# Kernel tuning notes

Measured on AMD Instinct MI355X. Metric: run time of the kernel, lower is better.

Reference implementation:

```python
import jax, jax.numpy as jnp
import numpy as np

N = 50000        # num_nodes
E = 800000       # num edges (avg degree 16)
R = 8            # num_relations
D_IN = 128       # input_dim
D_H = 128        # gnn_dim
D_OUT = 128      # embed_dim
NUM_DRUGS = 4000 # nodes with node_type == 0 used for pairing
P = 8192         # number of drug pairs (edge_filter columns)


def setup_inputs() -> dict:
    key = jax.random.key(0)
    ks = jax.random.split(key, 24)
    s = 0.05

    def w(k, shape):
        return jax.random.normal(k, shape, jnp.float32) * s

    inp = {
        "x": jax.random.normal(ks[0], (N, D_IN), jnp.float32),
        "edge_index": jax.random.randint(ks[1], (2, E), 0, N),
        "edge_type": jax.random.randint(ks[2], (E,), 0, R),
        "node_type": jax.random.randint(ks[3], (N,), 0, 2),
        "edge_filter": jax.random.randint(ks[4], (2, P), 0, NUM_DRUGS),
        # RGCN layer 1/2/3: per-relation weights, root weight, bias
        "W1": w(ks[5], (R, D_IN, D_H)), "root1": w(ks[6], (D_IN, D_H)), "b1": jnp.zeros((D_H,), jnp.float32),
        "W2": w(ks[7], (R, D_H, D_H)),  "root2": w(ks[8], (D_H, D_H)),  "b2": jnp.zeros((D_H,), jnp.float32),
        "W3": w(ks[9], (R, D_H, D_H)),  "root3": w(ks[10], (D_H, D_H)), "b3": jnp.zeros((D_H,), jnp.float32),
        # ComboMLP: Bilinear(d,d,d) + 3-layer MLP
        "bil_W": w(ks[11], (D_H, D_H, D_H)), "bil_b": jnp.zeros((D_H,), jnp.float32),
        "m1_W": w(ks[12], (D_H, D_H)), "m1_b": jnp.zeros((D_H,), jnp.float32),
        "m2_W": w(ks[13], (D_H, D_H)), "m2_b": jnp.zeros((D_H,), jnp.float32),
        "m3_W": w(ks[14], (D_H, D_OUT)), "m3_b": jnp.zeros((D_OUT,), jnp.float32),
    }
    return inp


def _rgcn_layer(x, src, dst, etype, W, root, b):
    # PyG RGCNConv with aggr='mean': per relation r, mean of neighbor
    # features over incoming rel-r edges, transformed by W[r]; plus root + bias.
    d = x.shape[1]
    msgs = x[src]                                   # [E, d] gather
    seg = dst * R + etype                           # per-(node, relation) segment id
    agg = jax.ops.segment_sum(msgs, seg, num_segments=N * R).reshape(N, R, d)
    cnt = jax.ops.segment_sum(jnp.ones_like(etype, jnp.float32), seg,
                              num_segments=N * R).reshape(N, R, 1)
    mean = agg / jnp.maximum(cnt, 1.0)              # nodes w/o rel-r edges -> 0
    return jnp.einsum('nrd,rde->ne', mean, W) + x @ root + b


def reference(x, edge_index, edge_type, node_type, edge_filter,
              W1, root1, b1, W2, root2, b2, W3, root3, b3,
              bil_W, bil_b, m1_W, m1_b, m2_W, m2_b, m3_W, m3_b):
    src, dst = edge_index[0], edge_index[1]
    h = jax.nn.relu(_rgcn_layer(x, src, dst, edge_type, W1, root1, b1))
    h = jax.nn.relu(_rgcn_layer(h, src, dst, edge_type, W2, root2, b2))
    h = jax.nn.relu(_rgcn_layer(h, src, dst, edge_type, W3, root3, b3))

    # drug_embeds = kg_out[where(node_type == 0)] (fixed-size for jit)
    drug_idx = jnp.nonzero(node_type == 0, size=NUM_DRUGS, fill_value=0)[0]
    drug = h[drug_idx]                              # [NUM_DRUGS, d]
    fa = drug[edge_filter[0]]                       # [P, d]
    fb = drug[edge_filter[1]]                       # [P, d]

    # torch.nn.Bilinear: out[p,o] = fa[p] @ bil_W[o] @ fb[p] + bil_b[o]
    x_ab = jax.nn.relu(jnp.einsum('pi,oij,pj->po', fa, bil_W, fb) + bil_b)
    x_ab = jax.nn.relu(x_ab @ m1_W + m1_b)
    x_ab = jax.nn.relu(x_ab @ m2_W + m2_b)
    return x_ab @ m3_W + m3_b                       # [P, D_OUT]
```

## Files before the change

kernel.cpp:

```cpp
#include <hip/hip_runtime.h>
#include <hip/hip_bf16.h>

typedef unsigned short ushort_t;
typedef __attribute__((ext_vector_type(8))) short short8v;
typedef __attribute__((ext_vector_type(4))) float f32x4;
typedef __attribute__((ext_vector_type(4))) int int4v;

#define NN 50000
#define EE 800000
#define RRR 8
#define DD 128
#define NDRUG 4000
#define PPAIR 8192
#define BML 32
#define AFS 1160

#define XB4   (NN * DD / 4)
#define WCAT1 (144 * 128 * 8)
#define PREP_T (XB4 + 3 * WCAT1 + 3 * 16384 + 2097152)

__device__ __forceinline__ float bf2f(ushort_t u) {
    unsigned int v = ((unsigned int)u) << 16;
    float f; __builtin_memcpy(&f, &v, 4); return f;
}
__device__ __forceinline__ ushort_t f2bf(float f) {
    unsigned int b; __builtin_memcpy(&b, &f, 4);
    unsigned int r = (b + 0x7FFFu + ((b >> 16) & 1u)) >> 16;
    return (ushort_t)r;
}
__device__ __forceinline__ unsigned int pkbf(float lo, float hi) {
    unsigned int r;
    asm("v_cvt_pk_bf16_f32 %0, %1, %2" : "=v"(r) : "v"(lo), "v"(hi));
    return r;
}

__global__ __launch_bounds__(256) void k_prep(
        const float* __restrict__ x,
        const float* __restrict__ W1, const float* __restrict__ r1,
        const float* __restrict__ W2, const float* __restrict__ r2,
        const float* __restrict__ W3, const float* __restrict__ r3,
        const float* __restrict__ m1W, const float* __restrict__ m2W,
        const float* __restrict__ m3W, const float* __restrict__ bilW,
        const int* __restrict__ ei, const int* __restrict__ et,
        ushort_t* __restrict__ xb,
        ushort_t* __restrict__ Wc1, ushort_t* __restrict__ Wc2, ushort_t* __restrict__ Wc3,
        ushort_t* __restrict__ mo1, ushort_t* __restrict__ mo2, ushort_t* __restrict__ mo3,
        ushort_t* __restrict__ Wb3, int* __restrict__ cnt) {
    int idx = blockIdx.x * 256 + threadIdx.x;
    if (idx < XB4) {
        float4 v = ((const float4*)x)[idx];
        uint2 o;
        o.x = (unsigned int)f2bf(v.x) | ((unsigned int)f2bf(v.y) << 16);
        o.y = (unsigned int)f2bf(v.z) | ((unsigned int)f2bf(v.w) << 16);
        ((uint2*)xb)[idx] = o;
    } else if (idx < XB4 + 3 * WCAT1) {
        int t = idx - XB4;
        int l = t / WCAT1, j = t - l * WCAT1;
        const float* W8   = (l == 0) ? W1 : (l == 1) ? W2 : W3;
        const float* root = (l == 0) ? r1 : (l == 1) ? r2 : r3;
        ushort_t* dst     = (l == 0) ? Wc1 : (l == 1) ? Wc2 : Wc3;
        int e = j & 7, col = (j >> 3) & 127, ko = j >> 10;
        int k = ko * 8 + e, slab = k >> 7, kk = k & 127;
        const float* src = (slab < 8) ? (W8 + slab * 16384) : root;
        dst[j] = f2bf(src[kk * 128 + col]);
    } else if (idx < XB4 + 3 * WCAT1 + 3 * 16384) {
        int t = idx - XB4 - 3 * WCAT1;
        int l = t >> 14, j = t & 16383;
        const float* src = (l == 0) ? m1W : (l == 1) ? m2W : m3W;
        ushort_t* dst    = (l == 0) ? mo1 : (l == 1) ? mo2 : mo3;
        int col = j >> 7, kk = j & 127;
        dst[j] = f2bf(src[kk * 128 + col]);
    } else if (idx < PREP_T) {
        int j = idx - (XB4 + 3 * WCAT1 + 3 * 16384);
        int e = j & 7, o = (j >> 3) & 127, ko = j >> 10;
        Wb3[j] = f2bf(bilW[(size_t)o * 16384 + ko * 8 + e]);
    } else {
        int e = idx - PREP_T;
        if (e < EE) {
            int dst = ei[EE + e];
            atomicAdd(&cnt[dst * RRR + et[e]], 1);
        }
    }
}

__global__ __launch_bounds__(1024) void k_scanA(const int* __restrict__ cnt,
                                                const int* __restrict__ ntype,
                                                float* __restrict__ inv,
                                                int* __restrict__ offs,
                                                int* __restrict__ selx,
                                                int* __restrict__ part,
                                                int* __restrict__ part2) {
    __shared__ int w1[16], w2[16];
    int tid = threadIdx.x, wid = tid >> 6, lane = tid & 63;
    int i = blockIdx.x * 1024 + tid;
    int a0 = 0, b0 = 0;
    if (i < NN) {
#pragma unroll
        for (int r = 0; r < RRR; r++) {
            int c = cnt[i * RRR + r];
            a0 += c;
            inv[i * RRR + r] = 1.0f / (float)(c > 0 ? c : 1);
        }
        b0 = (ntype[i] == 0) ? 1 : 0;
    }
    int a = a0, b = b0;
#pragma unroll
    for (int off = 1; off < 64; off <<= 1) {
        int ua = __shfl_up(a, off);
        int ub = __shfl_up(b, off);
        if (lane >= off) { a += ua; b += ub; }
    }
    if (lane == 63) { w1[wid] = a; w2[wid] = b; }
    __syncthreads();
    if (wid == 0) {
        int wa = (lane < 16) ? w1[lane] : 0;
        int wb = (lane < 16) ? w2[lane] : 0;
#pragma unroll
        for (int off = 1; off < 16; off <<= 1) {
            int ua = __shfl_up(wa, off);
            int ub = __shfl_up(wb, off);
            if (lane >= off) { wa += ua; wb += ub; }
        }
        if (lane < 16) { w1[lane] = wa; w2[lane] = wb; }
    }
    __syncthreads();
    if (i < NN) {
        offs[i] = (wid ? w1[wid - 1] : 0) + (a - a0);
        selx[i] = (wid ? w2[wid - 1] : 0) + (b - b0);
    }
    if (tid == 0) { part[blockIdx.x] = w1[15]; part2[blockIdx.x] = w2[15]; }
}

__global__ __launch_bounds__(64) void k_scanB(int* __restrict__ part,
                                              int* __restrict__ part2, int nPart) {
    int tid = threadIdx.x;
    int p0 = (tid < nPart) ? part[tid] : 0;
    int q0 = (tid < nPart) ? part2[tid] : 0;
    int p = p0, q = q0;
#pragma unroll
    for (int off = 1; off < 64; off <<= 1) {
        int u = __shfl_up(p, off);
        int v = __shfl_up(q, off);
        if (tid >= off) { p += u; q += v; }
    }
    if (tid < nPart) { part[tid] = p - p0; part2[tid] = q - q0; }
}

__global__ __launch_bounds__(1024) void k_scanC(int* __restrict__ offs,
                                                const int* __restrict__ selx,
                                                const int* __restrict__ part,
                                                const int* __restrict__ part2,
                                                const int* __restrict__ ntype,
                                                int* __restrict__ cursor,
                                                int* __restrict__ didx) {
    int i = blockIdx.x * 1024 + threadIdx.x;
    if (i < NN) {
        int v = offs[i] + part[blockIdx.x];
        offs[i] = v;
        cursor[i] = v;
        if (ntype[i] == 0) {
            int s = selx[i] + part2[blockIdx.x];
            if (s < NDRUG) didx[s] = i;
        }
    }
    if (i == NN) offs[NN] = EE;
}

__global__ __launch_bounds__(256) void k_scatter(const int* __restrict__ ei,
                                                 const int* __restrict__ et,
                                                 int* __restrict__ cursor,
                                                 int* __restrict__ sorted) {
    int e = blockIdx.x * 256 + threadIdx.x;
    if (e < EE) {
        int dst = ei[EE + e];
        int pos = atomicAdd(&cursor[dst], 1);
        sorted[pos] = ei[e] | (et[e] << 20);
    }
}

__global__ __launch_bounds__(512) void k_layer(const ushort_t* __restrict__ hin,
                                               const ushort_t* __restrict__ WcatT,
                                               const float* __restrict__ bias,
                                               const float* __restrict__ inv,
                                               const int* __restrict__ offs,
                                               const int* __restrict__ sorted,
                                               ushort_t* __restrict__ hout) {
    __shared__ short Af[BML * AFS];
    int tid = threadIdx.x;
    int n0 = blockIdx.x * BML;
    int node = tid >> 4, tsub = tid & 15;
    int n = n0 + node;

    float acc[8][8];
#pragma unroll
    for (int r = 0; r < 8; r++)
#pragma unroll
        for (int q = 0; q < 8; q++) acc[r][q] = 0.f;
    short8v hv = {0, 0, 0, 0, 0, 0, 0, 0};

    if (n < NN) {
        hv = ((const short8v*)hin)[(size_t)n * 16 + tsub];
        int e0 = offs[n], e1 = offs[n + 1];
        const int4v* hg = (const int4v*)hin;
        for (int e = e0; e < e1; e++) {
            int pk = sorted[e];
            int src = pk & 0xFFFFF;
            int et = pk >> 20;
            union { int4v v; short s[8]; } u;
            u.v = hg[(size_t)src * 16 + tsub];
            float v[8];
#pragma unroll
            for (int q = 0; q < 8; q++) v[q] = bf2f((ushort_t)u.s[q]);
#define CASE_R(R) case R: _Pragma("unroll") for (int q = 0; q < 8; q++) acc[R][q] += v[q]; break;
            switch (et) {
                CASE_R(0) CASE_R(1) CASE_R(2) CASE_R(3)
                CASE_R(4) CASE_R(5) CASE_R(6) CASE_R(7)
            }
#undef CASE_R
        }
    }
    int nc = (n < NN) ? n : (NN - 1);
#pragma unroll
    for (int slab = 0; slab < 8; slab++) {
        float sc = (n < NN) ? inv[nc * 8 + slab] : 0.f;
        union { unsigned int u[4]; short8v v; } cv;
        cv.u[0] = pkbf(acc[slab][0] * sc, acc[slab][1] * sc);
        cv.u[1] = pkbf(acc[slab][2] * sc, acc[slab][3] * sc);
        cv.u[2] = pkbf(acc[slab][4] * sc, acc[slab][5] * sc);
        cv.u[3] = pkbf(acc[slab][6] * sc, acc[slab][7] * sc);
        *(short8v*)&Af[node * AFS + slab * 128 + tsub * 8] = cv.v;
    }
    *(short8v*)&Af[node * AFS + 1024 + tsub * 8] = hv;
    __syncthreads();

    int wid = tid >> 6, lane = tid & 63, lo = lane & 15, hi = lane >> 4;
    int rhalf = wid & 1, cgrp = wid >> 1;
    int arow = rhalf * 16 + lo;
    f32x4 a0v = {0.f, 0.f, 0.f, 0.f}, a1v = {0.f, 0.f, 0.f, 0.f};
    const int4v* Bg = (const int4v*)WcatT;
#pragma unroll
    for (int kc = 0; kc < 9; kc++) {
#pragma unroll
        for (int s = 0; s < 4; s++) {
            short8v a = *(const short8v*)&Af[arow * AFS + kc * 128 + s * 32 + hi * 8];
            int ko = kc * 16 + s * 4 + hi;
            union { int4v i; short8v s8; } b0, b1;
            b0.i = Bg[ko * 128 + cgrp * 32 + lo];
            b1.i = Bg[ko * 128 + cgrp * 32 + 16 + lo];
            a0v = __builtin_amdgcn_mfma_f32_16x16x32_bf16(a, b0.s8, a0v, 0, 0, 0);
            a1v = __builtin_amdgcn_mfma_f32_16x16x32_bf16(a, b1.s8, a1v, 0, 0, 0);
        }
    }
#pragma unroll
    for (int q = 0; q < 4; q++) {
        int r = n0 + rhalf * 16 + hi * 4 + q;
        if (r < NN) {
            int c = cgrp * 32 + lo;
            float v0 = fmaxf(a0v[q] + bias[c], 0.f);
            float v1 = fmaxf(a1v[q] + bias[c + 16], 0.f);
            hout[(size_t)r * 128 + c] = f2bf(v0);
            hout[(size_t)r * 128 + c + 16] = f2bf(v1);
        }
    }
}

__global__ __launch_bounds__(256) void k_mfma_nn(const ushort_t* __restrict__ A,
                                                 const ushort_t* __restrict__ Wt,
                                                 const float* __restrict__ bias,
                                                 ushort_t* __restrict__ outb,
                                                 float* __restrict__ outf,
                                                 int M, int nMblk, int relu) {
    __shared__ short As[64 * 136];
    __shared__ short Bs[128 * 136];
    int tid = threadIdx.x;
    int mblk = blockIdx.x % nMblk;
    int row0 = mblk * 64;

    const int4v* Ag = (const int4v*)A;
    int4v* AsV = (int4v*)As;
    for (int idx = tid; idx < 1024; idx += 256) {
        int row = idx >> 4, ck = idx & 15;
        int grow = row0 + row;
        int4v v = {0, 0, 0, 0};
        if (grow < M) v = Ag[(size_t)grow * 16 + ck];
        AsV[row * 17 + ck] = v;
    }
    const int4v* Wg = (const int4v*)Wt;
    int4v* BsV = (int4v*)Bs;
    for (int idx = tid; idx < 2048; idx += 256) {
        int col = idx >> 4, ck = idx & 15;
        BsV[col * 17 + ck] = Wg[idx];
    }
    __syncthreads();

    int wid = tid >> 6, lane = tid & 63, lo = lane & 15, hi = lane >> 4;
    int wrow0 = wid * 16;
    f32x4 acc[8];
#pragma unroll
    for (int t = 0; t < 8; t++) acc[t] = (f32x4)(0.f);

#pragma unroll
    for (int s = 0; s < 4; ++s) {
        short8v a = *(const short8v*)&As[(wrow0 + lo) * 136 + s * 32 + hi * 8];
#pragma unroll
        for (int t = 0; t < 8; t++) {
            short8v b = *(const short8v*)&Bs[(t * 16 + lo) * 136 + s * 32 + hi * 8];
            acc[t] = __builtin_amdgcn_mfma_f32_16x16x32_bf16(a, b, acc[t], 0, 0, 0);
        }
    }

#pragma unroll
    for (int t = 0; t < 8; t++) {
        int col = t * 16 + lo;
        float bs = bias ? bias[col] : 0.f;
#pragma unroll
        for (int q = 0; q < 4; q++) {
            int grow = row0 + wrow0 + hi * 4 + q;
            if (grow < M) {
                float v = acc[t][q] + bs;
                if (relu) v = fmaxf(v, 0.f);
                size_t oidx = (size_t)grow * 128 + col;
                if (outb) outb[oidx] = f2bf(v);
                else      outf[oidx] = v;
            }
        }
    }
}

__global__ __launch_bounds__(512) void k_bil(const ushort_t* __restrict__ hb,
                                             const int* __restrict__ didx,
                                             const int* __restrict__ efil,
                                             const ushort_t* __restrict__ Wb,
                                             const float* __restrict__ bilb,
                                             ushort_t* __restrict__ xab) {
    __shared__ __align__(16) char smem[67072];
    __shared__ int pa[64], pb[64];
    float* faT = (float*)smem;
    float* fbF = (float*)(smem + 33280);
    int tid = threadIdx.x;
    int p0 = blockIdx.x * 64;

    if (tid < 64) pa[tid] = didx[efil[p0 + tid]];
    else if (tid < 128) pb[tid - 64] = didx[efil[PPAIR + p0 + tid - 64]];
    __syncthreads();

    for (int t = tid; t < 1024; t += 512) {
        int p = t >> 4, c8 = t & 15;
        const int4v* hg = (const int4v*)hb;
        union { int4v v; short s[8]; } ra, rb;
        ra.v = hg[(size_t)pa[p] * 16 + c8];
        rb.v = hg[(size_t)pb[p] * 16 + c8];
        float4* fb4 = (float4*)fbF;
        float4 f0, f1;
        f0.x = bf2f((ushort_t)rb.s[0]); f0.y = bf2f((ushort_t)rb.s[1]);
        f0.z = bf2f((ushort_t)rb.s[2]); f0.w = bf2f((ushort_t)rb.s[3]);
        f1.x = bf2f((ushort_t)rb.s[4]); f1.y = bf2f((ushort_t)rb.s[5]);
        f1.z = bf2f((ushort_t)rb.s[6]); f1.w = bf2f((ushort_t)rb.s[7]);
        fb4[p * 33 + c8 * 2] = f0;
        fb4[p * 33 + c8 * 2 + 1] = f1;
#pragma unroll
        for (int j = 0; j < 8; j++)
            faT[(c8 * 8 + j) * 65 + p] = bf2f((ushort_t)ra.s[j]);
    }
    __syncthreads();

    int wid = tid >> 6, lane = tid & 63, lo = lane & 15, hi = lane >> 4;
    int ph = wid & 1, kQ = wid >> 1;
    const int4v* Wbg = (const int4v*)Wb;
    const float4* fb4 = (const float4*)fbF;

    f32x4 acc0[8], acc1[8];
#pragma unroll
    for (int t = 0; t < 8; t++) { acc0[t] = (f32x4)(0.f); acc1[t] = (f32x4)(0.f); }

    for (int s = 0; s < 128; ++s) {
        int ko = (kQ << 9) + (s << 2) + hi;
        int4v braw[8];
#pragma unroll
        for (int t = 0; t < 8; t++)
            braw[t] = Wbg[ko * 128 + t * 16 + lo];

        int i = (kQ << 5) + (s >> 2);
        int jc4 = ((s & 3) << 3) + (hi << 1);
        short8v afr0, afr1;
#pragma unroll
        for (int mi = 0; mi < 2; ++mi) {
            int prow = (ph << 5) + (mi << 4) + lo;
            float fa = faT[i * 65 + prow];
            float4 f0 = fb4[prow * 33 + jc4];
            float4 f1 = fb4[prow * 33 + jc4 + 1];
            union { unsigned int u[4]; short8v v; } cv;
            cv.u[0] = pkbf(fa * f0.x, fa * f0.y);
            cv.u[1] = pkbf(fa * f0.z, fa * f0.w);
            cv.u[2] = pkbf(fa * f1.x, fa * f1.y);
            cv.u[3] = pkbf(fa * f1.z, fa * f1.w);
            if (mi == 0) afr0 = cv.v; else afr1 = cv.v;
        }
#pragma unroll
        for (int t = 0; t < 8; t++) {
            union { int4v i4; short8v s8; } bb; bb.i4 = braw[t];
            acc0[t] = __builtin_amdgcn_mfma_f32_16x16x32_bf16(afr0, bb.s8, acc0[t], 0, 0, 0);
            acc1[t] = __builtin_amdgcn_mfma_f32_16x16x32_bf16(afr1, bb.s8, acc1[t], 0, 0, 0);
        }
    }
    __syncthreads();

    float* redF = (float*)smem;
    if (kQ >= 2) {
        float* r = redF + (((kQ - 2) << 1) + ph) * 4096;
#pragma unroll
        for (int t = 0; t < 8; t++)
#pragma unroll
            for (int q = 0; q < 4; q++) {
                r[(hi * 4 + q) * 128 + t * 16 + lo] = acc0[t][q];
                r[(16 + hi * 4 + q) * 128 + t * 16 + lo] = acc1[t][q];
            }
    }
    __syncthreads();
    if (kQ < 2) {
        float* r = redF + ((kQ << 1) + ph) * 4096;
#pragma unroll
        for (int t = 0; t < 8; t++)
#pragma unroll
            for (int q = 0; q < 4; q++) {
                acc0[t][q] += r[(hi * 4 + q) * 128 + t * 16 + lo];
                acc1[t][q] += r[(16 + hi * 4 + q) * 128 + t * 16 + lo];
            }
    }
    __syncthreads();
    if (kQ == 1) {
        float* r = redF + ph * 4096;
#pragma unroll
        for (int t = 0; t < 8; t++)
#pragma unroll
            for (int q = 0; q < 4; q++) {
                r[(hi * 4 + q) * 128 + t * 16 + lo] = acc0[t][q];
                r[(16 + hi * 4 + q) * 128 + t * 16 + lo] = acc1[t][q];
            }
    }
    __syncthreads();
    if (kQ == 0) {
        float* r = redF + ph * 4096;
#pragma unroll
        for (int t = 0; t < 8; t++) {
            int col = t * 16 + lo;
            float bs = bilb[col];
#pragma unroll
            for (int q = 0; q < 4; q++) {
                float s0 = acc0[t][q] + r[(hi * 4 + q) * 128 + col] + bs;
                float s1 = acc1[t][q] + r[(16 + hi * 4 + q) * 128 + col] + bs;
                int pr0 = p0 + (ph << 5) + hi * 4 + q;
                int pr1 = pr0 + 16;
                xab[(size_t)pr0 * 128 + col] = f2bf(fmaxf(s0, 0.f));
                xab[(size_t)pr1 * 128 + col] = f2bf(fmaxf(s1, 0.f));
            }
        }
    }
}


extern "C" void kernel_launch(void* const* d_in, const int* in_sizes, int n_in,
                              void* d_out, int out_size, void* d_ws, size_t ws_size,
                              hipStream_t stream) {
    const float* x      = (const float*)d_in[0];
    const int*   ei     = (const int*)d_in[1];
    const int*   et     = (const int*)d_in[2];
    const int*   ntype  = (const int*)d_in[3];
    const int*   efil   = (const int*)d_in[4];
    const float* W1 = (const float*)d_in[5];
    const float* r1 = (const float*)d_in[6];
    const float* b1 = (const float*)d_in[7];
    const float* W2 = (const float*)d_in[8];
    const float* r2 = (const float*)d_in[9];
    const float* b2 = (const float*)d_in[10];
    const float* W3 = (const float*)d_in[11];
    const float* r3 = (const float*)d_in[12];
    const float* b3 = (const float*)d_in[13];
    const float* bilW = (const float*)d_in[14];
    const float* bilb = (const float*)d_in[15];
    const float* m1W = (const float*)d_in[16];
    const float* m1b = (const float*)d_in[17];
    const float* m2W = (const float*)d_in[18];
    const float* m2b = (const float*)d_in[19];
    const float* m3W = (const float*)d_in[20];
    const float* m3b = (const float*)d_in[21];
    float* outp = (float*)d_out;

    char* ws = (char*)d_ws;
    size_t off = 0;
    auto alloc = [&](size_t bytes) { size_t c = off; off = (off + bytes + 255) & ~(size_t)255; return c; };

    const int nScanBlk = (NN + 1023) / 1024;

    size_t oxb   = alloc((size_t)NN * 128 * 2);
    size_t ohA   = alloc((size_t)NN * 128 * 2);
    size_t ohB   = alloc((size_t)NN * 128 * 2);
    size_t oWc1  = alloc((size_t)WCAT1 * 2);
    size_t oWc2  = alloc((size_t)WCAT1 * 2);
    size_t oWc3  = alloc((size_t)WCAT1 * 2);
    size_t omW1  = alloc((size_t)16384 * 2);
    size_t omW2  = alloc((size_t)16384 * 2);
    size_t omW3  = alloc((size_t)16384 * 2);
    size_t oWb   = alloc((size_t)2097152 * 2);
    size_t oxab1 = alloc((size_t)PPAIR * 128 * 2);
    size_t oxab2 = alloc((size_t)PPAIR * 128 * 2);
    size_t ocnt  = alloc((size_t)NN * RRR * sizeof(int));
    size_t odidx = alloc((size_t)NDRUG * sizeof(int));
    size_t oinv  = alloc((size_t)NN * RRR * sizeof(float));
    size_t ooffs = alloc((size_t)(NN + 1) * sizeof(int));
    size_t oselx = alloc((size_t)NN * sizeof(int));
    size_t ocur  = alloc((size_t)NN * sizeof(int));
    size_t opart = alloc((size_t)64 * sizeof(int));
    size_t opart2 = alloc((size_t)64 * sizeof(int));
    size_t osort = alloc((size_t)EE * sizeof(int));

    ushort_t* xb   = (ushort_t*)(ws + oxb);
    ushort_t* hbA  = (ushort_t*)(ws + ohA);
    ushort_t* hbB  = (ushort_t*)(ws + ohB);
    ushort_t* Wc1  = (ushort_t*)(ws + oWc1);
    ushort_t* Wc2  = (ushort_t*)(ws + oWc2);
    ushort_t* Wc3  = (ushort_t*)(ws + oWc3);
    ushort_t* mWt1 = (ushort_t*)(ws + omW1);
    ushort_t* mWt2 = (ushort_t*)(ws + omW2);
    ushort_t* mWt3 = (ushort_t*)(ws + omW3);
    ushort_t* Wb3  = (ushort_t*)(ws + oWb);
    ushort_t* xab1 = (ushort_t*)(ws + oxab1);
    ushort_t* xab2 = (ushort_t*)(ws + oxab2);
    int*      cnt  = (int*)(ws + ocnt);
    int*      didx = (int*)(ws + odidx);
    float*    inv  = (float*)(ws + oinv);
    int*      offs = (int*)(ws + ooffs);
    int*      selx = (int*)(ws + oselx);
    int*      cursor = (int*)(ws + ocur);
    int*      part = (int*)(ws + opart);
    int*      part2 = (int*)(ws + opart2);
    int*      sorted = (int*)(ws + osort);

    hipMemsetAsync(cnt, 0, (odidx - ocnt) + (size_t)NDRUG * sizeof(int), stream);

    k_prep<<<(PREP_T + EE + 255) / 256, 256, 0, stream>>>(
        x, W1, r1, W2, r2, W3, r3, m1W, m2W, m3W, bilW, ei, et,
        xb, Wc1, Wc2, Wc3, mWt1, mWt2, mWt3, Wb3, cnt);

    k_scanA<<<nScanBlk, 1024, 0, stream>>>(cnt, ntype, inv, offs, selx, part, part2);
    k_scanB<<<1, 64, 0, stream>>>(part, part2, nScanBlk);
    k_scanC<<<nScanBlk + 1, 1024, 0, stream>>>(offs, selx, part, part2, ntype, cursor, didx);
    k_scatter<<<(EE + 255) / 256, 256, 0, stream>>>(ei, et, cursor, sorted);

    const int NBL = (NN + BML - 1) / BML;

    k_layer<<<NBL, 512, 0, stream>>>(xb,  Wc1, b1, inv, offs, sorted, hbA);
    k_layer<<<NBL, 512, 0, stream>>>(hbA, Wc2, b2, inv, offs, sorted, hbB);
    k_layer<<<NBL, 512, 0, stream>>>(hbB, Wc3, b3, inv, offs, sorted, hbA);

    k_bil<<<PPAIR / 64, 512, 0, stream>>>(hbA, didx, efil, Wb3, bilb, xab1);
    const int nMblkP = PPAIR / 64;
    k_mfma_nn<<<nMblkP, 256, 0, stream>>>(xab1, mWt1, m1b, xab2, nullptr, PPAIR, nMblkP, 1);
    k_mfma_nn<<<nMblkP, 256, 0, stream>>>(xab2, mWt2, m2b, xab1, nullptr, PPAIR, nMblkP, 1);
    k_mfma_nn<<<nMblkP, 256, 0, stream>>>(xab1, mWt3, m3b, nullptr, outp, PPAIR, nMblkP, 0);
}
```

Measured before the change: 719.0 us.

## Split bilinear kernel across K halves and smaller pair tiles with reduction pass

The bilinear kernel now processes 32 pairs per block instead of 64. It also splits the 16384-long reduction dimension into two halves across blocks, raising the grid from 128 to 512 blocks so more compute units are occupied. Each block reduces its 8 waves' partials in shared memory and writes fp32 partial sums to a workspace. A new elementwise kernel adds the two halves, applies bias and ReLU, and stores bf16. The cost is roughly double the bilinear weight traffic, extra fp32 partial writes and reads, and one more kernel launch.

```diff
diff --git a/kernel.cpp b/kernel.cpp
--- a/kernel.cpp
+++ b/kernel.cpp
@@ -331,21 +331,22 @@
                                              const int* __restrict__ didx,
                                              const int* __restrict__ efil,
                                              const ushort_t* __restrict__ Wb,
-                                             const float* __restrict__ bilb,
-                                             ushort_t* __restrict__ xab) {
-    __shared__ __align__(16) char smem[67072];
-    __shared__ int pa[64], pb[64];
+                                             float* __restrict__ partial) {
+    __shared__ __align__(16) char smem[65536];
+    __shared__ int pa[32], pb[32];
     float* faT = (float*)smem;
-    float* fbF = (float*)(smem + 33280);
+    float* fbF = (float*)(smem + 16896);
     int tid = threadIdx.x;
-    int p0 = blockIdx.x * 64;
-
-    if (tid < 64) pa[tid] = didx[efil[p0 + tid]];
-    else if (tid < 128) pb[tid - 64] = didx[efil[PPAIR + p0 + tid - 64]];
-    __syncthreads();
-
-    for (int t = tid; t < 1024; t += 512) {
-        int p = t >> 4, c8 = t & 15;
+    int pt = blockIdx.x & 255;
+    int kh = blockIdx.x >> 8;
+    int p0 = pt * 32;
+
+    if (tid < 32) pa[tid] = didx[efil[p0 + tid]];
+    else if (tid < 64) pb[tid - 32] = didx[efil[PPAIR + p0 + tid - 32]];
+    __syncthreads();
+
+    {
+        int p = tid >> 4, c8 = tid & 15;
         const int4v* hg = (const int4v*)hb;
         union { int4v v; short s[8]; } ra, rb;
         ra.v = hg[(size_t)pa[p] * 16 + c8];
@@ -360,12 +361,11 @@
         fb4[p * 33 + c8 * 2 + 1] = f1;
 #pragma unroll
         for (int j = 0; j < 8; j++)
-            faT[(c8 * 8 + j) * 65 + p] = bf2f((ushort_t)ra.s[j]);
+            faT[(c8 * 8 + j) * 33 + p] = bf2f((ushort_t)ra.s[j]);
     }
     __syncthreads();
 
     int wid = tid >> 6, lane = tid & 63, lo = lane & 15, hi = lane >> 4;
-    int ph = wid & 1, kQ = wid >> 1;
     const int4v* Wbg = (const int4v*)Wb;
     const float4* fb4 = (const float4*)fbF;
 
@@ -373,20 +373,20 @@
 #pragma unroll
     for (int t = 0; t < 8; t++) { acc0[t] = (f32x4)(0.f); acc1[t] = (f32x4)(0.f); }
 
-    for (int s = 0; s < 128; ++s) {
-        int ko = (kQ << 9) + (s << 2) + hi;
+    for (int s = 0; s < 32; ++s) {
+        int ko = (kh << 10) + (wid << 7) + (s << 2) + hi;
         int4v braw[8];
 #pragma unroll
         for (int t = 0; t < 8; t++)
             braw[t] = Wbg[ko * 128 + t * 16 + lo];
 
-        int i = (kQ << 5) + (s >> 2);
+        int i = (kh << 6) + (wid << 3) + (s >> 2);
         int jc4 = ((s & 3) << 3) + (hi << 1);
         short8v afr0, afr1;
 #pragma unroll
         for (int mi = 0; mi < 2; ++mi) {
-            int prow = (ph << 5) + (mi << 4) + lo;
-            float fa = faT[i * 65 + prow];
+            int prow = (mi << 4) + lo;
+            float fa = faT[i * 33 + prow];
             float4 f0 = fb4[prow * 33 + jc4];
             float4 f1 = fb4[prow * 33 + jc4 + 1];
             union { unsigned int u[4]; short8v v; } cv;
@@ -406,8 +406,8 @@
     __syncthreads();
 
     float* redF = (float*)smem;
-    if (kQ >= 2) {
-        float* r = redF + (((kQ - 2) << 1) + ph) * 4096;
+    if (wid >= 4) {
+        float* r = redF + (wid - 4) * 4096;
 #pragma unroll
         for (int t = 0; t < 8; t++)
 #pragma unroll
@@ -417,8 +417,8 @@
             }
     }
     __syncthreads();
-    if (kQ < 2) {
-        float* r = redF + ((kQ << 1) + ph) * 4096;
+    if (wid < 4) {
+        float* r = redF + wid * 4096;
 #pragma unroll
         for (int t = 0; t < 8; t++)
 #pragma unroll
@@ -428,8 +428,8 @@
             }
     }
     __syncthreads();
-    if (kQ == 1) {
-        float* r = redF + ph * 4096;
+    if (wid < 4) {
+        float* r = redF + wid * 4096;
 #pragma unroll
         for (int t = 0; t < 8; t++)
 #pragma unroll
@@ -439,22 +439,19 @@
             }
     }
     __syncthreads();
-    if (kQ == 0) {
-        float* r = redF + ph * 4096;
-#pragma unroll
-        for (int t = 0; t < 8; t++) {
-            int col = t * 16 + lo;
-            float bs = bilb[col];
-#pragma unroll
-            for (int q = 0; q < 4; q++) {
-                float s0 = acc0[t][q] + r[(hi * 4 + q) * 128 + col] + bs;
-                float s1 = acc1[t][q] + r[(16 + hi * 4 + q) * 128 + col] + bs;
-                int pr0 = p0 + (ph << 5) + hi * 4 + q;
-                int pr1 = pr0 + 16;
-                xab[(size_t)pr0 * 128 + col] = f2bf(fmaxf(s0, 0.f));
-                xab[(size_t)pr1 * 128 + col] = f2bf(fmaxf(s1, 0.f));
-            }
-        }
+    float* dst = partial + ((size_t)kh * PPAIR + p0) * 128;
+    for (int idx = tid; idx < 4096; idx += 512) {
+        dst[idx] = redF[idx] + redF[4096 + idx] + redF[8192 + idx] + redF[12288 + idx];
+    }
+}
+
+__global__ __launch_bounds__(256) void k_bilred(const float* __restrict__ partial,
+                                                const float* __restrict__ bilb,
+                                                ushort_t* __restrict__ xab) {
+    int idx = blockIdx.x * 256 + threadIdx.x;
+    if (idx < PPAIR * 128) {
+        float s = partial[idx] + partial[PPAIR * 128 + idx] + bilb[idx & 127];
+        xab[idx] = f2bf(fmaxf(s, 0.f));
     }
 }
 
@@ -504,6 +501,7 @@
     size_t oWb   = alloc((size_t)2097152 * 2);
     size_t oxab1 = alloc((size_t)PPAIR * 128 * 2);
     size_t oxab2 = alloc((size_t)PPAIR * 128 * 2);
+    size_t opbil = alloc((size_t)2 * PPAIR * 128 * sizeof(float));
     size_t ocnt  = alloc((size_t)NN * RRR * sizeof(int));
     size_t odidx = alloc((size_t)NDRUG * sizeof(int));
     size_t oinv  = alloc((size_t)NN * RRR * sizeof(float));
@@ -526,6 +524,7 @@
     ushort_t* Wb3  = (ushort_t*)(ws + oWb);
     ushort_t* xab1 = (ushort_t*)(ws + oxab1);
     ushort_t* xab2 = (ushort_t*)(ws + oxab2);
+    float*    pbil = (float*)(ws + opbil);
     int*      cnt  = (int*)(ws + ocnt);
     int*      didx = (int*)(ws + odidx);
     float*    inv  = (float*)(ws + oinv);
@@ -553,7 +552,8 @@
     k_layer<<<NBL, 512, 0, stream>>>(hbA, Wc2, b2, inv, offs, sorted, hbB);
     k_layer<<<NBL, 512, 0, stream>>>(hbB, Wc3, b3, inv, offs, sorted, hbA);
 
-    k_bil<<<PPAIR / 64, 512, 0, stream>>>(hbA, didx, efil, Wb3, bilb, xab1);
+    k_bil<<<512, 512, 0, stream>>>(hbA, didx, efil, Wb3, pbil);
+    k_bilred<<<(PPAIR * 128 + 255) / 256, 256, 0, stream>>>(pbil, bilb, xab1);
     const int nMblkP = PPAIR / 64;
     k_mfma_nn<<<nMblkP, 256, 0, stream>>>(xab1, mWt1, m1b, xab2, nullptr, PPAIR, nMblkP, 1);
     k_mfma_nn<<<nMblkP, 256, 0, stream>>>(xab2, mWt2, m2b, xab1, nullptr, PPAIR, nMblkP, 1);
```

After: 618.6 us. 14.0% less time.
